# Kernel optimization log

Measured on AMD Instinct MI355X. Metric: run time of the kernel, lower is better.

## Reference

```python
import jax, jax.numpy as jnp
import numpy as np


def setup_inputs() -> dict:
    key = jax.random.key(0)
    ks = jax.random.split(key, 6)
    B, T, C, H, E = 4, 2048, 768, 3072, 16
    scale = 0.02
    return {
        "x": jax.random.normal(ks[0], (B, T, C), dtype=jnp.float32),
        "w_shared_fc": jax.random.normal(ks[1], (C, 2 * H), dtype=jnp.float32) * scale,
        "w_shared_proj": jax.random.normal(ks[2], (H, C), dtype=jnp.float32) * scale,
        "w_experts_fc": jax.random.normal(ks[3], (E, C, 2 * H), dtype=jnp.float32) * scale,
        "w_experts_proj": jax.random.normal(ks[4], (E, H, C), dtype=jnp.float32) * scale,
        "w_gate": jax.random.normal(ks[5], (C, E), dtype=jnp.float32) * scale,
        "expert_bias": jnp.zeros((E,), dtype=jnp.float32),
        "top_k": 4,
    }


def _swiglu(h):
    gate, val = jnp.split(h, 2, axis=-1)
    return jax.nn.silu(gate) * val


def reference(x, w_shared_fc, w_shared_proj, w_experts_fc, w_experts_proj,
              w_gate, expert_bias, top_k):
    B, T, C = x.shape
    E = expert_bias.shape[0]
    N = B * T

    # shared expert (applied to every token)
    shared = _swiglu(x @ w_shared_fc) @ w_shared_proj  # [B,T,C]

    # top-k sigmoid routing
    gate_logits = x @ w_gate + expert_bias            # [B,T,E]
    gate_w = jax.nn.sigmoid(gate_logits)
    top_w, top_idx = jax.lax.top_k(gate_w, top_k)     # [B,T,K]
    top_w = top_w / jnp.sum(top_w, axis=-1, keepdims=True)

    # dense per-token/per-expert weight matrix [N,E] (zero for unrouted)
    w_dense = jnp.sum(jax.nn.one_hot(top_idx, E, dtype=x.dtype) * top_w[..., None],
                      axis=-2).reshape(N, E)

    flat_x = x.reshape(N, C)

    def body(acc, params):
        wfc, wproj, we = params  # [C,2H], [H,C], [N]
        out = _swiglu(flat_x @ wfc) @ wproj  # [N,C]
        return acc + we[:, None] * out, None

    routed, _ = jax.lax.scan(body, jnp.zeros_like(flat_x),
                             (w_experts_fc, w_experts_proj, w_dense.T))
    return shared + routed.reshape(B, T, C)
```

## Files before the change

### kernel.cpp

```cpp
#include <hip/hip_runtime.h>
#include <hip/hip_bf16.h>

typedef __hip_bfloat16 bf16;
typedef __attribute__((ext_vector_type(8))) short short8;
typedef __attribute__((ext_vector_type(4))) float float4v;

#define BK 32

__device__ __forceinline__ void gload16(const bf16* g, bf16* s) {
    __builtin_amdgcn_global_load_lds(
        (const __attribute__((address_space(1))) void*)g,
        (__attribute__((address_space(3))) void*)s, 16, 0, 0);
}


__global__ void k_convert_x(const float* __restrict__ in, bf16* __restrict__ out,
                            int n, int* __restrict__ cnt) {
    if (blockIdx.x == 0 && threadIdx.x < 16) cnt[threadIdx.x] = 0;
    int i = (blockIdx.x * blockDim.x + threadIdx.x) * 4;
    if (i + 3 < n) {
        float4 v = *(const float4*)(in + i);
        out[i + 0] = __float2bfloat16(v.x);
        out[i + 1] = __float2bfloat16(v.y);
        out[i + 2] = __float2bfloat16(v.z);
        out[i + 3] = __float2bfloat16(v.w);
    }
}

__global__ __launch_bounds__(256) void k_transpose64(
    const float* __restrict__ in, bf16* __restrict__ out, int R, int S) {
    __shared__ float tile[64][65];
    size_t mat = (size_t)blockIdx.z * R * S;
    int s0 = blockIdx.x * 64, r0 = blockIdx.y * 64;
    int tid = threadIdx.x;
    int rr = tid >> 4, sc = (tid & 15) * 4;
    #pragma unroll
    for (int i = 0; i < 4; ++i) {
        float4 v = *(const float4*)(in + mat + (size_t)(r0 + rr + i * 16) * S + s0 + sc);
        tile[rr + i * 16][sc + 0] = v.x;
        tile[rr + i * 16][sc + 1] = v.y;
        tile[rr + i * 16][sc + 2] = v.z;
        tile[rr + i * 16][sc + 3] = v.w;
    }
    __syncthreads();
    int ss = tid >> 3, rc = (tid & 7) * 8;
    #pragma unroll
    for (int i = 0; i < 2; ++i) {
        int s = ss + i * 32;
        bf16 tmp[8];
        #pragma unroll
        for (int j = 0; j < 8; ++j) tmp[j] = __float2bfloat16(tile[rc + j][s]);
        *(uint4*)(out + mat + (size_t)(s0 + s) * R + r0 + rc) = *(uint4*)tmp;
    }
}

__global__ void k_gate(const float* __restrict__ x, const float* __restrict__ wg,
                       const float* __restrict__ bias, int* __restrict__ cnt,
                       int* __restrict__ tok, float* __restrict__ wl,
                       int* __restrict__ slotk) {
    __shared__ float gates[16][17];
    int t = threadIdx.x;
    int tl = t >> 4;
    int e = t & 15;
    int token = blockIdx.x * 16 + tl;
    const float* xr = x + (size_t)token * 768;
    float acc = 0.f;
    #pragma unroll 4
    for (int c = 0; c < 768; ++c) acc += xr[c] * wg[c * 16 + e];
    acc += bias[e];
    gates[tl][e] = 1.f / (1.f + expf(-acc));
    __syncthreads();
    if (t < 16) {
        int token2 = blockIdx.x * 16 + t;
        float g[16];
        #pragma unroll
        for (int j = 0; j < 16; ++j) g[j] = gates[t][j];
        int idx[4]; float w[4]; float sum = 0.f;
        #pragma unroll
        for (int k = 0; k < 4; ++k) {
            float best = -1e30f; int bi = 0;
            #pragma unroll
            for (int j = 0; j < 16; ++j)
                if (g[j] > best) { best = g[j]; bi = j; }
            idx[k] = bi; w[k] = best; sum += best; g[bi] = -1e30f;
        }
        float inv = 1.f / sum;
        for (int k = 0; k < 4; ++k) {
            int slot = atomicAdd(&cnt[idx[k]], 1);
            tok[(idx[k] << 13) + slot] = token2;
            wl[(idx[k] << 13) + slot] = w[k] * inv;
            slotk[token2 * 4 + k] = (idx[k] << 13) | slot;
        }
    }
}

__global__ void k_offsets(const int* __restrict__ cnt, int* __restrict__ offs) {
    if (threadIdx.x == 0) {
        int s = 0;
        for (int e = 0; e < 16; ++e) { offs[e] = s; s += cnt[e]; }
    }
}

__global__ __launch_bounds__(192) void k_combine(
    const float* __restrict__ routed, const int* __restrict__ slotk,
    const int* __restrict__ offs, float* __restrict__ out) {
    int t = blockIdx.x;
    int c4 = threadIdx.x * 4;
    float* op = out + (size_t)t * 768 + c4;
    float4 acc = *(float4*)op;
    #pragma unroll
    for (int k = 0; k < 4; ++k) {
        int sk = slotk[t * 4 + k];
        int e = sk >> 13, sl = sk & 8191;
        const float* row = routed + (size_t)(offs[e] + sl) * 768 + c4;
        float4 v = *(const float4*)row;
        acc.x += v.x; acc.y += v.y; acc.z += v.z; acc.w += v.w;
    }
    *(float4*)op = acc;
}

template<int GATHER>
__device__ __forceinline__ void fc_body(
    const bf16* __restrict__ A, const bf16* __restrict__ BT,
    bf16* __restrict__ act, const int* __restrict__ cnt,
    const int* __restrict__ offs, const int* __restrict__ tok) {
    const int Kd = 768, H = 3072;
    int e = blockIdx.z;
    int m0 = blockIdx.y * 128;
    int n0 = blockIdx.x * 128;
    int M;
    size_t actbase = 0;
    const int* tl = nullptr;
    if (GATHER) {
        M = cnt[e];
        if (m0 >= M) return;
        tl = tok + (e << 13);
        actbase = (size_t)offs[e] * H;
        BT += (size_t)e * 6144 * Kd;
    } else {
        M = 8192;
    }

    __shared__ bf16 sA[128 * BK];
    __shared__ bf16 sBg[128 * BK];
    __shared__ bf16 sBv[128 * BK];

    int tid = threadIdx.x;
    int lane = tid & 63;
    int w = tid >> 6;
    int wm = w & 1, wn = w >> 1;

    int sr = tid >> 2;
    int k2 = (tid & 3) ^ ((sr >> 1) & 3);

    int grA = GATHER ? tl[min(m0 + sr, M - 1)] : (m0 + sr);
    const bf16* gA  = A  + (size_t)grA * Kd + k2 * 8;
    const bf16* gBg = BT + (size_t)(n0 + sr) * Kd + k2 * 8;
    const bf16* gBv = BT + (size_t)(H + n0 + sr) * Kd + k2 * 8;
    bf16* sAp  = sA  + tid * 8;
    bf16* sBgp = sBg + tid * 8;
    bf16* sBvp = sBv + tid * 8;

    float4v ag[4][2] = {};
    float4v av[4][2] = {};
    int quad = lane >> 4, l16 = lane & 15;
    int q2 = quad ^ ((l16 >> 1) & 3);

    for (int k0 = 0; k0 < Kd; k0 += BK) {
        __syncthreads();
        gload16(gA + k0, sAp);
        gload16(gBg + k0, sBgp);
        gload16(gBv + k0, sBvp);
        __syncthreads();
        short8 af[4], bg[2], bv[2];
        #pragma unroll
        for (int mf = 0; mf < 4; ++mf) {
            int row = wm * 64 + mf * 16 + l16;
            af[mf] = *(const short8*)(sA + row * BK + q2 * 8);
        }
        #pragma unroll
        for (int nf = 0; nf < 2; ++nf) {
            int row = wn * 32 + nf * 16 + l16;
            bg[nf] = *(const short8*)(sBg + row * BK + q2 * 8);
            bv[nf] = *(const short8*)(sBv + row * BK + q2 * 8);
        }
        #pragma unroll
        for (int mf = 0; mf < 4; ++mf)
            #pragma unroll
            for (int nf = 0; nf < 2; ++nf) {
                ag[mf][nf] = __builtin_amdgcn_mfma_f32_16x16x32_bf16(af[mf], bg[nf], ag[mf][nf], 0, 0, 0);
                av[mf][nf] = __builtin_amdgcn_mfma_f32_16x16x32_bf16(af[mf], bv[nf], av[mf][nf], 0, 0, 0);
            }
    }

    #pragma unroll
    for (int mf = 0; mf < 4; ++mf)
        #pragma unroll
        for (int nf = 0; nf < 2; ++nf)
            #pragma unroll
            for (int r = 0; r < 4; ++r) {
                int mrow = m0 + wm * 64 + mf * 16 + quad * 4 + r;
                if (GATHER && mrow >= M) continue;
                int col = n0 + wn * 32 + nf * 16 + l16;
                float g = ag[mf][nf][r];
                float v = av[mf][nf][r];
                float sg = g / (1.f + __expf(-g));
                act[actbase + (size_t)mrow * H + col] = __float2bfloat16(sg * v);
            }
}

__global__ __launch_bounds__(512) void k_fc_shared(
    const bf16* __restrict__ A, const bf16* __restrict__ BT, bf16* __restrict__ act,
    const int* __restrict__ cnt, const int* __restrict__ offs, const int* __restrict__ tok) {
    fc_body<0>(A, BT, act, cnt, offs, tok);
}
__global__ __launch_bounds__(512) void k_fc_routed(
    const bf16* __restrict__ A, const bf16* __restrict__ BT, bf16* __restrict__ act,
    const int* __restrict__ cnt, const int* __restrict__ offs, const int* __restrict__ tok) {
    fc_body<1>(A, BT, act, cnt, offs, tok);
}

template<int ROUTED>
__device__ __forceinline__ void proj_body(
    const bf16* __restrict__ Aact, const bf16* __restrict__ PT,
    float* __restrict__ out, const int* __restrict__ cnt,
    const int* __restrict__ offs, const float* __restrict__ wl) {
    const int Kd = 3072;
    int e = blockIdx.z;
    int m0 = blockIdx.y * 256;
    int n0 = blockIdx.x * 128;
    int M;
    size_t abase = 0;
    int roffs = 0;
    if (ROUTED) {
        M = cnt[e];
        if (m0 >= M) return;
        roffs = offs[e];
        abase = (size_t)roffs * Kd;
        PT += (size_t)e * 768 * Kd;
    } else {
        M = 8192;
    }

    __shared__ bf16 sA[256 * BK];
    __shared__ bf16 sB[128 * BK];

    int tid = threadIdx.x, lane = tid & 63, w = tid >> 6;
    int wm = w & 3, wn = w >> 2;

    int srA0 = tid >> 2;
    int srA1 = (tid + 512) >> 2;
    int k2A0 = (tid & 3) ^ ((srA0 >> 1) & 3);
    int k2A1 = (tid & 3) ^ ((srA1 >> 1) & 3);
    int srB = tid >> 2;
    int k2B = (tid & 3) ^ ((srB >> 1) & 3);

    int ra0 = min(m0 + srA0, M - 1);
    int ra1 = min(m0 + srA1, M - 1);
    const bf16* gA0 = Aact + abase + (size_t)ra0 * Kd + k2A0 * 8;
    const bf16* gA1 = Aact + abase + (size_t)ra1 * Kd + k2A1 * 8;
    const bf16* gB  = PT + (size_t)(n0 + srB) * Kd + k2B * 8;
    bf16* sA0p = sA + tid * 8;
    bf16* sA1p = sA + (tid + 512) * 8;
    bf16* sBp  = sB + tid * 8;

    float4v acc[4][4] = {};
    int quad = lane >> 4, l16 = lane & 15;
    int q2 = quad ^ ((l16 >> 1) & 3);

    for (int kk = 0; kk < Kd; kk += BK) {
        __syncthreads();
        gload16(gA0 + kk, sA0p);
        gload16(gA1 + kk, sA1p);
        gload16(gB + kk, sBp);
        __syncthreads();
        short8 af[4], bb[4];
        #pragma unroll
        for (int i = 0; i < 4; ++i) {
            int rowa = wm * 64 + i * 16 + l16;
            int rowb = wn * 64 + i * 16 + l16;
            af[i] = *(const short8*)(sA + rowa * BK + q2 * 8);
            bb[i] = *(const short8*)(sB + rowb * BK + q2 * 8);
        }
        #pragma unroll
        for (int mf = 0; mf < 4; ++mf)
            #pragma unroll
            for (int nf = 0; nf < 4; ++nf)
                acc[mf][nf] = __builtin_amdgcn_mfma_f32_16x16x32_bf16(af[mf], bb[nf], acc[mf][nf], 0, 0, 0);
    }

    #pragma unroll
    for (int mf = 0; mf < 4; ++mf) {
        #pragma unroll
        for (int r = 0; r < 4; ++r) {
            int mr = m0 + wm * 64 + mf * 16 + quad * 4 + r;
            if (ROUTED) {
                if (mr < M) {
                    float wgt = wl[(e << 13) + mr];
                    float* orow = out + (size_t)(roffs + mr) * 768;
                    #pragma unroll
                    for (int nf = 0; nf < 4; ++nf) {
                        int col = n0 + wn * 64 + nf * 16 + l16;
                        orow[col] = wgt * acc[mf][nf][r];
                    }
                }
            } else {
                #pragma unroll
                for (int nf = 0; nf < 4; ++nf) {
                    int col = n0 + wn * 64 + nf * 16 + l16;
                    out[(size_t)mr * 768 + col] = acc[mf][nf][r];
                }
            }
        }
    }
}

__global__ __launch_bounds__(512) void k_proj_shared(
    const bf16* __restrict__ Aact, const bf16* __restrict__ PT, float* __restrict__ out,
    const int* __restrict__ cnt, const int* __restrict__ offs, const float* __restrict__ wl) {
    proj_body<0>(Aact, PT, out, cnt, offs, wl);
}
__global__ __launch_bounds__(512) void k_proj_routed(
    const bf16* __restrict__ Aact, const bf16* __restrict__ PT, float* __restrict__ out,
    const int* __restrict__ cnt, const int* __restrict__ offs, const float* __restrict__ wl) {
    proj_body<1>(Aact, PT, out, cnt, offs, wl);
}


extern "C" void kernel_launch(void* const* d_in, const int* in_sizes, int n_in,
                              void* d_out, int out_size, void* d_ws, size_t ws_size,
                              hipStream_t stream) {
    const float* x    = (const float*)d_in[0];
    const float* wfc  = (const float*)d_in[1];
    const float* wpr  = (const float*)d_in[2];
    const float* wefc = (const float*)d_in[3];
    const float* wepr = (const float*)d_in[4];
    const float* wg   = (const float*)d_in[5];
    const float* eb   = (const float*)d_in[6];
    float* out = (float*)d_out;

    char* p = (char*)d_ws;
    bf16* x_bf  = (bf16*)p; p += (size_t)8192 * 768 * 2;
    bf16* fcT_s = (bf16*)p; p += (size_t)6144 * 768 * 2;
    bf16* prT_s = (bf16*)p; p += (size_t)768 * 3072 * 2;
    bf16* fcT_e = (bf16*)p; p += (size_t)16 * 6144 * 768 * 2;
    bf16* prT_e = (bf16*)p; p += (size_t)16 * 768 * 3072 * 2;
    bf16* act_s = (bf16*)p; p += (size_t)8192 * 3072 * 2;
    bf16* act_r = (bf16*)p; p += (size_t)32768 * 3072 * 2;
    int* cnt    = (int*)p;  p += 64;
    int* offs   = (int*)p;  p += 64;
    int* tok    = (int*)p;  p += (size_t)16 * 8192 * 4;
    float* wl   = (float*)p; p += (size_t)16 * 8192 * 4;
    int* slotk  = (int*)p;  p += (size_t)8192 * 4 * 4;
    float* routed_out = (float*)fcT_e;

    k_convert_x<<<dim3(6144), dim3(256), 0, stream>>>(x, x_bf, 8192 * 768, cnt);
    k_transpose64<<<dim3(96, 12, 1), dim3(256), 0, stream>>>(wfc, fcT_s, 768, 6144);
    k_transpose64<<<dim3(12, 48, 1), dim3(256), 0, stream>>>(wpr, prT_s, 3072, 768);
    k_transpose64<<<dim3(96, 12, 16), dim3(256), 0, stream>>>(wefc, fcT_e, 768, 6144);
    k_transpose64<<<dim3(12, 48, 16), dim3(256), 0, stream>>>(wepr, prT_e, 3072, 768);
    k_gate<<<dim3(512), dim3(256), 0, stream>>>(x, wg, eb, cnt, tok, wl, slotk);
    k_offsets<<<dim3(1), dim3(64), 0, stream>>>(cnt, offs);

    k_fc_shared<<<dim3(24, 64, 1), dim3(512), 0, stream>>>(x_bf, fcT_s, act_s, cnt, offs, tok);
    k_fc_routed<<<dim3(24, 64, 16), dim3(512), 0, stream>>>(x_bf, fcT_e, act_r, cnt, offs, tok);
    k_proj_shared<<<dim3(6, 32, 1), dim3(512), 0, stream>>>(act_s, prT_s, out, cnt, offs, wl);
    k_proj_routed<<<dim3(6, 32, 16), dim3(512), 0, stream>>>(act_r, prT_e, routed_out, cnt, offs, wl);
    k_combine<<<dim3(8192), dim3(192), 0, stream>>>(routed_out, slotk, offs, out);
}
```

Before: 1.636 ms.

## Rewrite FC GEMM with 256x256 tiles, double-buffered LDS and interleaved gate/value weights

The FC GEMMs now use 256x256 output tiles with BK=64, a double-buffered LDS pipeline that prefetches the next k-tile while issuing MFMAs, and s_setprio around the compute phases. The transpose kernel interleaves the gate and value halves of the fc weights in 16-column groups, so a single B tile holds both and the SwiGLU pairs land in adjacent accumulator fragments. The aim is more data reuse per LDS load and overlap of global loads with MFMA work. The cost is much higher register and LDS use (128 KB LDS, 128 accumulators per thread), which lowers occupancy. The larger M tile also wastes more work on partially filled expert tiles.

```diff
diff --git a/kernel.cpp b/kernel.cpp
--- a/kernel.cpp
+++ b/kernel.cpp
@@ -12,6 +12,8 @@
         (const __attribute__((address_space(1))) void*)g,
         (__attribute__((address_space(3))) void*)s, 16, 0, 0);
 }
+
+#define BAR() do { asm volatile("" ::: "memory"); __builtin_amdgcn_s_barrier(); asm volatile("" ::: "memory"); } while (0)
 
 
 __global__ void k_convert_x(const float* __restrict__ in, bf16* __restrict__ out,
@@ -28,7 +30,7 @@
 }
 
 __global__ __launch_bounds__(256) void k_transpose64(
-    const float* __restrict__ in, bf16* __restrict__ out, int R, int S) {
+    const float* __restrict__ in, bf16* __restrict__ out, int R, int S, int fuse) {
     __shared__ float tile[64][65];
     size_t mat = (size_t)blockIdx.z * R * S;
     int s0 = blockIdx.x * 64, r0 = blockIdx.y * 64;
@@ -46,11 +48,18 @@
     int ss = tid >> 3, rc = (tid & 7) * 8;
     #pragma unroll
     for (int i = 0; i < 2; ++i) {
-        int s = ss + i * 32;
+        int sl = ss + i * 32;
+        int sg = s0 + sl;
+        int so = sg;
+        if (fuse) {
+            int half = (sg >= 3072) ? 1 : 0;
+            int idx = sg - half * 3072;
+            so = ((idx >> 4) << 5) | (half << 4) | (idx & 15);
+        }
         bf16 tmp[8];
         #pragma unroll
-        for (int j = 0; j < 8; ++j) tmp[j] = __float2bfloat16(tile[rc + j][s]);
-        *(uint4*)(out + mat + (size_t)(s0 + s) * R + r0 + rc) = *(uint4*)tmp;
+        for (int j = 0; j < 8; ++j) tmp[j] = __float2bfloat16(tile[rc + j][sl]);
+        *(uint4*)(out + mat + (size_t)so * R + r0 + rc) = *(uint4*)tmp;
     }
 }
 
@@ -120,17 +129,16 @@
 }
 
 template<int GATHER>
-__device__ __forceinline__ void fc_body(
+__device__ __forceinline__ void fc8_body(
     const bf16* __restrict__ A, const bf16* __restrict__ BT,
     bf16* __restrict__ act, const int* __restrict__ cnt,
-    const int* __restrict__ offs, const int* __restrict__ tok) {
+    const int* __restrict__ offs, const int* __restrict__ tok)
+{
     const int Kd = 768, H = 3072;
     int e = blockIdx.z;
-    int m0 = blockIdx.y * 128;
-    int n0 = blockIdx.x * 128;
-    int M;
-    size_t actbase = 0;
-    const int* tl = nullptr;
+    int m0 = blockIdx.y * 256;
+    int n0 = blockIdx.x * 256;
+    int M; size_t actbase = 0; const int* tl = nullptr;
     if (GATHER) {
         M = cnt[e];
         if (m0 >= M) return;
@@ -141,69 +149,135 @@
         M = 8192;
     }
 
-    __shared__ bf16 sA[128 * BK];
-    __shared__ bf16 sBg[128 * BK];
-    __shared__ bf16 sBv[128 * BK];
+    __shared__ bf16 lds[65536];
 
     int tid = threadIdx.x;
     int lane = tid & 63;
     int w = tid >> 6;
     int wm = w & 1, wn = w >> 1;
-
-    int sr = tid >> 2;
-    int k2 = (tid & 3) ^ ((sr >> 1) & 3);
-
-    int grA = GATHER ? tl[min(m0 + sr, M - 1)] : (m0 + sr);
-    const bf16* gA  = A  + (size_t)grA * Kd + k2 * 8;
-    const bf16* gBg = BT + (size_t)(n0 + sr) * Kd + k2 * 8;
-    const bf16* gBv = BT + (size_t)(H + n0 + sr) * Kd + k2 * 8;
-    bf16* sAp  = sA  + tid * 8;
-    bf16* sBgp = sBg + tid * 8;
-    bf16* sBvp = sBv + tid * 8;
-
-    float4v ag[4][2] = {};
-    float4v av[4][2] = {};
     int quad = lane >> 4, l16 = lane & 15;
-    int q2 = quad ^ ((l16 >> 1) & 3);
-
-    for (int k0 = 0; k0 < Kd; k0 += BK) {
-        __syncthreads();
-        gload16(gA + k0, sAp);
-        gload16(gBg + k0, sBgp);
-        gload16(gBv + k0, sBvp);
-        __syncthreads();
-        short8 af[4], bg[2], bv[2];
-        #pragma unroll
-        for (int mf = 0; mf < 4; ++mf) {
-            int row = wm * 64 + mf * 16 + l16;
-            af[mf] = *(const short8*)(sA + row * BK + q2 * 8);
-        }
-        #pragma unroll
-        for (int nf = 0; nf < 2; ++nf) {
-            int row = wn * 32 + nf * 16 + l16;
-            bg[nf] = *(const short8*)(sBg + row * BK + q2 * 8);
-            bv[nf] = *(const short8*)(sBv + row * BK + q2 * 8);
-        }
-        #pragma unroll
-        for (int mf = 0; mf < 4; ++mf)
-            #pragma unroll
-            for (int nf = 0; nf < 2; ++nf) {
-                ag[mf][nf] = __builtin_amdgcn_mfma_f32_16x16x32_bf16(af[mf], bg[nf], ag[mf][nf], 0, 0, 0);
-                av[mf][nf] = __builtin_amdgcn_mfma_f32_16x16x32_bf16(af[mf], bv[nf], av[mf][nf], 0, 0, 0);
-            }
-    }
-
-    #pragma unroll
-    for (int mf = 0; mf < 4; ++mf)
-        #pragma unroll
-        for (int nf = 0; nf < 2; ++nf)
+
+    int srow = tid >> 3;
+    int g0 = (tid & 7) ^ (srow & 7);
+
+    const bf16* gA[2][2]; const bf16* gB[2][2];
+    #pragma unroll
+    for (int h = 0; h < 2; ++h) {
+        int ra = m0 + h * 128 + srow;
+        int rb = n0 + h * 128 + srow;
+        int a0 = GATHER ? tl[min(ra, M - 1)] : ra;
+        int a1 = GATHER ? tl[min(ra + 64, M - 1)] : (ra + 64);
+        gA[h][0] = A + (size_t)a0 * Kd + g0 * 8;
+        gA[h][1] = A + (size_t)a1 * Kd + g0 * 8;
+        gB[h][0] = BT + (size_t)rb * Kd + g0 * 8;
+        gB[h][1] = BT + (size_t)(rb + 64) * Kd + g0 * 8;
+    }
+
+    auto stageA = [&](int buf, int kt) {
+        bf16* d = lds + buf * 32768;
+        gload16(gA[0][0] + kt * 64, d + tid * 8);
+        gload16(gA[0][1] + kt * 64, d + (tid + 512) * 8);
+        gload16(gA[1][0] + kt * 64, d + 8192 + tid * 8);
+        gload16(gA[1][1] + kt * 64, d + 8192 + (tid + 512) * 8);
+    };
+    auto stageB = [&](int buf, int kt) {
+        bf16* d = lds + buf * 32768 + 16384;
+        gload16(gB[0][0] + kt * 64, d + tid * 8);
+        gload16(gB[0][1] + kt * 64, d + (tid + 512) * 8);
+        gload16(gB[1][0] + kt * 64, d + 8192 + tid * 8);
+        gload16(gB[1][1] + kt * 64, d + 8192 + (tid + 512) * 8);
+    };
+
+    int swz0 = ((quad    ) ^ (l16 & 7)) * 8;
+    int swz1 = ((quad | 4) ^ (l16 & 7)) * 8;
+    int aBase = wm * 8192 + l16 * 64;
+    int bBase = 16384 + wn * 4096 + l16 * 64;
+
+    float4v acc[8][4] = {};
+
+    stageA(0, 0);
+    stageB(0, 0);
+    asm volatile("s_waitcnt vmcnt(0)" ::: "memory");
+    BAR();
+
+    for (int t = 0; t < 12; ++t) {
+        const bf16* cb = lds + (t & 1) * 32768;
+        int nb = (t & 1) ^ 1;
+        bool pf = (t < 11);
+        short8 ar[4], br[4];
+
+        #pragma unroll
+        for (int nf = 0; nf < 4; ++nf)
+            br[nf] = *(const short8*)(cb + bBase + nf * 1024 + swz0);
+        #pragma unroll
+        for (int mf = 0; mf < 4; ++mf)
+            ar[mf] = *(const short8*)(cb + aBase + mf * 1024 + swz0);
+        if (pf) stageA(nb, t + 1);
+        __builtin_amdgcn_s_setprio(1);
+        #pragma unroll
+        for (int mf = 0; mf < 4; ++mf)
+            #pragma unroll
+            for (int nf = 0; nf < 4; ++nf)
+                acc[mf][nf] = __builtin_amdgcn_mfma_f32_16x16x32_bf16(ar[mf], br[nf], acc[mf][nf], 0, 0, 0);
+        __builtin_amdgcn_s_setprio(0);
+        BAR();
+
+        #pragma unroll
+        for (int mf = 0; mf < 4; ++mf)
+            ar[mf] = *(const short8*)(cb + aBase + (mf + 4) * 1024 + swz0);
+        if (pf) stageB(nb, t + 1);
+        __builtin_amdgcn_s_setprio(1);
+        #pragma unroll
+        for (int mf = 0; mf < 4; ++mf)
+            #pragma unroll
+            for (int nf = 0; nf < 4; ++nf)
+                acc[mf + 4][nf] = __builtin_amdgcn_mfma_f32_16x16x32_bf16(ar[mf], br[nf], acc[mf + 4][nf], 0, 0, 0);
+        __builtin_amdgcn_s_setprio(0);
+        asm volatile("s_waitcnt vmcnt(4)" ::: "memory");
+        BAR();
+
+        #pragma unroll
+        for (int nf = 0; nf < 4; ++nf)
+            br[nf] = *(const short8*)(cb + bBase + nf * 1024 + swz1);
+        #pragma unroll
+        for (int mf = 0; mf < 4; ++mf)
+            ar[mf] = *(const short8*)(cb + aBase + mf * 1024 + swz1);
+        __builtin_amdgcn_s_setprio(1);
+        #pragma unroll
+        for (int mf = 0; mf < 4; ++mf)
+            #pragma unroll
+            for (int nf = 0; nf < 4; ++nf)
+                acc[mf][nf] = __builtin_amdgcn_mfma_f32_16x16x32_bf16(ar[mf], br[nf], acc[mf][nf], 0, 0, 0);
+        __builtin_amdgcn_s_setprio(0);
+        BAR();
+
+        #pragma unroll
+        for (int mf = 0; mf < 4; ++mf)
+            ar[mf] = *(const short8*)(cb + aBase + (mf + 4) * 1024 + swz1);
+        __builtin_amdgcn_s_setprio(1);
+        #pragma unroll
+        for (int mf = 0; mf < 4; ++mf)
+            #pragma unroll
+            for (int nf = 0; nf < 4; ++nf)
+                acc[mf + 4][nf] = __builtin_amdgcn_mfma_f32_16x16x32_bf16(ar[mf], br[nf], acc[mf + 4][nf], 0, 0, 0);
+        __builtin_amdgcn_s_setprio(0);
+        asm volatile("s_waitcnt vmcnt(0)" ::: "memory");
+        BAR();
+    }
+
+    int orow = m0 + wm * 128;
+    int ocol = (n0 + wn * 64) >> 1;
+    #pragma unroll
+    for (int mf = 0; mf < 8; ++mf)
+        #pragma unroll
+        for (int j = 0; j < 2; ++j)
             #pragma unroll
             for (int r = 0; r < 4; ++r) {
-                int mrow = m0 + wm * 64 + mf * 16 + quad * 4 + r;
+                int mrow = orow + mf * 16 + quad * 4 + r;
                 if (GATHER && mrow >= M) continue;
-                int col = n0 + wn * 32 + nf * 16 + l16;
-                float g = ag[mf][nf][r];
-                float v = av[mf][nf][r];
+                int col = ocol + j * 16 + l16;
+                float g = acc[mf][2 * j][r];
+                float v = acc[mf][2 * j + 1][r];
                 float sg = g / (1.f + __expf(-g));
                 act[actbase + (size_t)mrow * H + col] = __float2bfloat16(sg * v);
             }
@@ -212,12 +286,12 @@
 __global__ __launch_bounds__(512) void k_fc_shared(
     const bf16* __restrict__ A, const bf16* __restrict__ BT, bf16* __restrict__ act,
     const int* __restrict__ cnt, const int* __restrict__ offs, const int* __restrict__ tok) {
-    fc_body<0>(A, BT, act, cnt, offs, tok);
+    fc8_body<0>(A, BT, act, cnt, offs, tok);
 }
 __global__ __launch_bounds__(512) void k_fc_routed(
     const bf16* __restrict__ A, const bf16* __restrict__ BT, bf16* __restrict__ act,
     const int* __restrict__ cnt, const int* __restrict__ offs, const int* __restrict__ tok) {
-    fc_body<1>(A, BT, act, cnt, offs, tok);
+    fc8_body<1>(A, BT, act, cnt, offs, tok);
 }
 
 template<int ROUTED>
@@ -355,15 +429,15 @@
     float* routed_out = (float*)fcT_e;
 
     k_convert_x<<<dim3(6144), dim3(256), 0, stream>>>(x, x_bf, 8192 * 768, cnt);
-    k_transpose64<<<dim3(96, 12, 1), dim3(256), 0, stream>>>(wfc, fcT_s, 768, 6144);
-    k_transpose64<<<dim3(12, 48, 1), dim3(256), 0, stream>>>(wpr, prT_s, 3072, 768);
-    k_transpose64<<<dim3(96, 12, 16), dim3(256), 0, stream>>>(wefc, fcT_e, 768, 6144);
-    k_transpose64<<<dim3(12, 48, 16), dim3(256), 0, stream>>>(wepr, prT_e, 3072, 768);
+    k_transpose64<<<dim3(96, 12, 1), dim3(256), 0, stream>>>(wfc, fcT_s, 768, 6144, 1);
+    k_transpose64<<<dim3(12, 48, 1), dim3(256), 0, stream>>>(wpr, prT_s, 3072, 768, 0);
+    k_transpose64<<<dim3(96, 12, 16), dim3(256), 0, stream>>>(wefc, fcT_e, 768, 6144, 1);
+    k_transpose64<<<dim3(12, 48, 16), dim3(256), 0, stream>>>(wepr, prT_e, 3072, 768, 0);
     k_gate<<<dim3(512), dim3(256), 0, stream>>>(x, wg, eb, cnt, tok, wl, slotk);
     k_offsets<<<dim3(1), dim3(64), 0, stream>>>(cnt, offs);
 
-    k_fc_shared<<<dim3(24, 64, 1), dim3(512), 0, stream>>>(x_bf, fcT_s, act_s, cnt, offs, tok);
-    k_fc_routed<<<dim3(24, 64, 16), dim3(512), 0, stream>>>(x_bf, fcT_e, act_r, cnt, offs, tok);
+    k_fc_shared<<<dim3(24, 32, 1), dim3(512), 0, stream>>>(x_bf, fcT_s, act_s, cnt, offs, tok);
+    k_fc_routed<<<dim3(24, 32, 16), dim3(512), 0, stream>>>(x_bf, fcT_e, act_r, cnt, offs, tok);
     k_proj_shared<<<dim3(6, 32, 1), dim3(512), 0, stream>>>(act_s, prT_s, out, cnt, offs, wl);
     k_proj_routed<<<dim3(6, 32, 16), dim3(512), 0, stream>>>(act_r, prT_e, routed_out, cnt, offs, wl);
     k_combine<<<dim3(8192), dim3(192), 0, stream>>>(routed_out, slotk, offs, out);
```

After: 1.597 ms. 1.02x faster.
